# Kernel optimization log

Hardware: AMD Instinct MI355X
Metric: run time of the kernel (lower is better)

## Reference

```python
import jax, jax.numpy as jnp
import numpy as np

NUM = 8          # k_f*k_f - 1 neighbors (k_f = 3)
IDX_REF = 4      # center position index among the 9 kernel positions
EPS_TGASS = 1e-8


def _bilinear_gather(img, iy, ix):
    """img: (B,C,H,W); iy, ix: (B,N) absolute pixel coords.
    Bilinear sampling with zero padding. Matches both F.grid_sample
    (align_corners=True, padding_mode='zeros') and 1x1 modulated deform conv."""
    B, C, H, W = img.shape
    y0 = jnp.floor(iy)
    x0 = jnp.floor(ix)
    wy1 = iy - y0
    wx1 = ix - x0
    out = jnp.zeros((B, C, iy.shape[1]), img.dtype)
    for dy, dx, wy, wx in ((0.0, 0.0, 1.0 - wy1, 1.0 - wx1),
                           (0.0, 1.0, 1.0 - wy1, wx1),
                           (1.0, 0.0, wy1, 1.0 - wx1),
                           (1.0, 1.0, wy1, wx1)):
        yc = y0 + dy
        xc = x0 + dx
        valid = ((yc >= 0) & (yc <= H - 1) & (xc >= 0) & (xc <= W - 1)).astype(img.dtype)
        yi = jnp.clip(yc, 0, H - 1).astype(jnp.int32)
        xi = jnp.clip(xc, 0, W - 1).astype(jnp.int32)
        v = jax.vmap(lambda im, y, x: im[:, y, x])(img, yi, xi)  # (B,C,N)
        out = out + v * (wy * wx * valid)[:, None, :]
    return out


def setup_inputs() -> dict:
    key = jax.random.key(0)
    ks = jax.random.split(key, 5)
    B, Cg, H, W = 4, 16, 384, 384
    num, Cf = NUM, NUM  # cos-affinity path requires fea channels == num neighbors
    guidance = jax.random.normal(ks[0], (B, Cg, H, W), jnp.float32)
    gt_depth_conf = jax.random.uniform(ks[1], (B, 1, H, W), dtype=jnp.float32)
    tgtimg_fea = jax.random.normal(ks[2], (B, Cf, H, W), jnp.float32)
    # offset/affinity conv: 3*num output channels, 3x3 kernel; small init so offsets span a few pixels
    W_oa = jax.random.normal(ks[3], (3 * num, Cg, 3, 3), jnp.float32) * 0.05
    b_oa = jax.random.normal(ks[4], (3 * num,), jnp.float32) * 0.05
    aff_scale_const = jnp.full((1,), 0.5 * num, jnp.float32)  # TGASS: gamma * num
    return {"guidance": guidance, "gt_depth_conf": gt_depth_conf,
            "tgtimg_fea": tgtimg_fea, "W_oa": W_oa, "b_oa": b_oa,
            "aff_scale_const": aff_scale_const}


def reference(guidance, gt_depth_conf, tgtimg_fea, W_oa, b_oa, aff_scale_const):
    B, Cg, H, W = guidance.shape
    num = NUM

    # offset + affinity prediction conv (3x3, SAME padding)
    offset_aff = jax.lax.conv_general_dilated(
        guidance, W_oa, (1, 1), 'SAME',
        dimension_numbers=('NCHW', 'OIHW', 'NCHW')) + b_oa[None, :, None, None]
    o1, o2, aff = jnp.split(offset_aff, 3, axis=1)            # each (B,num,H,W)
    offset = jnp.concatenate([o1, o2], axis=1).reshape(B, num, 2, H, W)

    # ---- cos affinity: grid-sample gather of (detached) target features at offset locations
    fea = jax.lax.stop_gradient(tgtimg_fea)                   # (B,C,H,W), C == num
    C = fea.shape[1]
    rows = jnp.broadcast_to(jnp.arange(H, dtype=offset.dtype)[:, None], (H, W))
    cols = jnp.broadcast_to(jnp.arange(W, dtype=offset.dtype)[None, :], (H, W))
    xy = jnp.stack([rows, cols], -1)                          # (H,W,2)
    xy = jnp.repeat(xy, num, axis=-1)                         # (H,W,2*num): rows*num then cols*num
    xy_off = offset.reshape(B, 2 * num, H, W).transpose(0, 2, 3, 1) + xy  # (B,H,W,2*num)
    xy_off = xy_off.reshape(B, H, W, num, 2)
    gx = 2.0 * xy_off[..., 0] / (W - 1) - 1.0                 # grid x (width) coord
    gy = 2.0 * xy_off[..., 1] / (H - 1) - 1.0                 # grid y (height) coord
    ix = (gx + 1.0) * (W - 1) / 2.0
    iy = (gy + 1.0) * (H - 1) / 2.0
    sampled = _bilinear_gather(fea, iy.reshape(B, -1), ix.reshape(B, -1))  # (B,C,H*W*num)
    # torch does a raw .reshape of the (B,C,H,W*num) grid_sample output
    offset_feas = sampled.reshape(B, C, H, W * num).reshape(B, H, W, num, C)
    offset_feas = offset_feas.transpose(0, 3, 1, 2, 4)        # (B,num,H,W,C)
    cos_w = (offset_feas * fea[:, :, :, :, None]).sum(axis=1).transpose(0, 3, 1, 2)  # (B,num,H,W)
    aff = aff * cos_w                                         # use_aff=True

    # TGASS scaling
    aff = jnp.tanh(aff) / (aff_scale_const + EPS_TGASS)

    # full offset tensor with a zero offset inserted for the reference (center) pixel
    zero = jnp.zeros((B, 1, 2, H, W), offset.dtype)
    offset_full = jnp.concatenate([offset[:, :IDX_REF], zero, offset[:, IDX_REF:]], 1)
    offset_out = offset_full.reshape(B, -1, H, W)             # (B, 2*(num+1), H, W)

    # confidence propagation: 1x1 deformable sample of depth confidence (offsets detached)
    offs = jax.lax.stop_gradient(offset)                      # (B,num,2,H,W)
    dy = offs[:, :, 0]
    dx = offs[:, :, 1]
    sy = dy + jnp.arange(H, dtype=dy.dtype)[None, None, :, None]
    sx = dx + jnp.arange(W, dtype=dx.dtype)[None, None, None, :]
    conf = _bilinear_gather(gt_depth_conf, sy.reshape(B, -1), sx.reshape(B, -1))
    conf_aff = conf.reshape(B, num, H, W)
    aff = aff * conf_aff

    # affinity normalization (TGASS branch)
    aff_abs_sum = jnp.abs(aff).sum(axis=1, keepdims=True) + 1e-4
    aff_abs_sum = jnp.maximum(aff_abs_sum, 1.0)
    aff = aff / aff_abs_sum
    aff_ref = 1.0 - aff.sum(axis=1, keepdims=True)
    aff_full = jnp.concatenate([aff[:, :IDX_REF], aff_ref, aff[:, IDX_REF:]], 1)  # (B,9,H,W)
    aff_full = jax.nn.softmax(aff_full, axis=1)
    return (offset_out, aff_full)
```

## Files before the change

### kernel.cpp

```cpp
#include <hip/hip_runtime.h>

constexpr int Bn = 4, CG = 16, HH = 384, WW = 384;
constexpr int HWSZ = HH * WW;
constexpr int COUT = 24;
constexpr int TSX = 32, TSY = 16;

__global__ void wtrans_kernel(const float* __restrict__ Wc,
                              float* __restrict__ Wt) {
  int i = blockIdx.x * 256 + threadIdx.x;
  if (i < COUT * CG * 9) {
    int oc = i / (CG * 9), rem = i % (CG * 9);
    Wt[rem * COUT + oc] = Wc[i];
  }
}

__global__ __launch_bounds__(256) void conv5_kernel(
    const float* __restrict__ g, const float* __restrict__ Wt,
    const float* __restrict__ bc, float* __restrict__ out_off,
    float* __restrict__ affc, float* __restrict__ offT3f) {
  __shared__ float lds[8 * 18 * 34];
  int bi = blockIdx.x;
  int bx = (bi % (WW / TSX)) * TSX;
  int by = ((bi / (WW / TSX)) % (HH / TSY)) * TSY;
  int b = bi / ((WW / TSX) * (HH / TSY));
  const float* gb = g + (size_t)b * CG * HWSZ;

  int t = threadIdx.x;
  int tx = t & 15, ty = t >> 4;
  float acc0[COUT], acc1[COUT];
#pragma unroll
  for (int oc = 0; oc < COUT; ++oc) {
    float bv = bc[oc];
    acc0[oc] = bv;
    acc1[oc] = bv;
  }

  for (int half = 0; half < 2; ++half) {
    if (half) __syncthreads();
    for (int k = t; k < 8 * 18 * 34; k += 256) {
      int icl = k / 612, rem = k - 612 * icl;
      int y = rem / 34, x = rem - 34 * y;
      int gy = by + y - 1, gx = bx + x - 1;
      float v = (gy >= 0 && gy < HH && gx >= 0 && gx < WW)
                    ? gb[(half * 8 + icl) * HWSZ + gy * WW + gx]
                    : 0.f;
      lds[k] = v;
    }
    __syncthreads();

    for (int icl = 0; icl < 8; ++icl) {
      int ic = half * 8 + icl;
      const float* base = lds + icl * 612 + ty * 34 + 2 * tx;
      float vals[3][4];
#pragma unroll
      for (int r = 0; r < 3; ++r) {
        float2 v01 = *(const float2*)(base + r * 34);
        float2 v23 = *(const float2*)(base + r * 34 + 2);
        vals[r][0] = v01.x;
        vals[r][1] = v01.y;
        vals[r][2] = v23.x;
        vals[r][3] = v23.y;
      }
#pragma unroll
      for (int r = 0; r < 3; ++r) {
#pragma unroll
        for (int c3 = 0; c3 < 3; ++c3) {
          float va = vals[r][c3], vb = vals[r][c3 + 1];
          const float* wp = Wt + (ic * 9 + r * 3 + c3) * COUT;
#pragma unroll
          for (int oc = 0; oc < COUT; ++oc) {
            acc0[oc] += va * wp[oc];
            acc1[oc] += vb * wp[oc];
          }
        }
      }
    }
  }

  int p = (by + ty) * WW + bx + 2 * tx;
  float* ob = out_off + (size_t)b * 18 * HWSZ;
#pragma unroll
  for (int c = 0; c < 16; ++c) {
    int c18 = (c < 8) ? c : c + 2;
    *(float2*)(ob + c18 * HWSZ + p) = make_float2(acc0[c], acc1[c]);
  }
  *(float2*)(ob + 8 * HWSZ + p) = make_float2(0.f, 0.f);
  *(float2*)(ob + 9 * HWSZ + p) = make_float2(0.f, 0.f);
  float* ab = affc + (size_t)b * 8 * HWSZ;
#pragma unroll
  for (int c = 0; c < 8; ++c)
    *(float2*)(ab + c * HWSZ + p) = make_float2(acc0[16 + c], acc1[16 + c]);

  {
    int X0 = bx + 2 * tx;
    int m = X0 >> 3, j = X0 & 7;
    int Lp = by + ty;
    float* o3b = offT3f + (size_t)b * 16 * 48 * 384 * 4;
#pragma unroll
    for (int pl = 0; pl < 8; ++pl) {
      int cp = pl >> 1, sel = pl & 1;
      int q = sel * 2 + (j >> 2);
      size_t di = ((size_t)(cp * 4 + q) * 48 + m) * 384 + Lp;
      *(float2*)(o3b + di * 4 + (j & 3)) =
          make_float2(acc0[8 + pl], acc1[8 + pl]);
    }
  }
}

__device__ __forceinline__ float bilin_zero(const float* __restrict__ img,
                                            float iy, float ix) {
  float y0f = floorf(iy), x0f = floorf(ix);
  float wy1 = iy - y0f, wx1 = ix - x0f;
  int y0 = (int)y0f, x0 = (int)x0f;
  float acc = 0.f;
#pragma unroll
  for (int dy = 0; dy < 2; ++dy) {
    int yc = y0 + dy;
    bool vy = (yc >= 0) && (yc <= HH - 1);
    int yi = min(max(yc, 0), HH - 1);
    float wy = dy ? wy1 : 1.f - wy1;
#pragma unroll
    for (int dx = 0; dx < 2; ++dx) {
      int xc = x0 + dx;
      bool vx = (xc >= 0) && (xc <= WW - 1);
      int xi = min(max(xc, 0), WW - 1);
      float wx = dx ? wx1 : 1.f - wx1;
      float v = img[yi * WW + xi];
      acc += v * (wy * wx) * ((vy && vx) ? 1.f : 0.f);
    }
  }
  return acc;
}

__global__ __launch_bounds__(256, 4) void cw47h_kernel(
    const float* __restrict__ fea, const float4* __restrict__ offT3,
    float* __restrict__ cw4) {
  __shared__ float patch[64][68];
  __shared__ float sfea[8][64][5];
  __shared__ float scw[4][64][5];
  int t = threadIdx.x;
  int lane = t & 63, wv = t >> 6;
  int bi = blockIdx.x;
  int Lblk = bi % 6;  bi /= 6;
  int mblk = bi % 12; bi /= 12;
  int a = bi % 8, b = bi / 8;
  int m = mblk * 4 + wv;

  const float* feab = fea + (size_t)b * 8 * HWSZ;
  const float* imgA = feab + (size_t)a * HWSZ;
  int p_base = a * 18432 + 48 * (Lblk * 64) + mblk * 4;

  int R0 = 32 * mblk - 12;
  R0 = (R0 < 0) ? 0 : (R0 > 320 ? 320 : R0);

#pragma unroll
  for (int i = 0; i < 2; ++i) {
    int L = i * 256 + t;
    int j = L >> 6, Lpl = L & 63;
    float4 v = *(const float4*)(feab + (size_t)j * HWSZ + p_base + 48 * Lpl);
    sfea[j][Lpl][0] = v.x;
    sfea[j][Lpl][1] = v.y;
    sfea[j][Lpl][2] = v.z;
    sfea[j][Lpl][3] = v.w;
  }
  {
    int row = t >> 4, colq = t & 15;
#pragma unroll
    for (int pass = 0; pass < 4; ++pass) {
      int r = pass * 16 + row;
      float4 v = *(const float4*)(imgA + (R0 + r) * WW + R0 + 4 * colq);
      *(float4*)&patch[r][4 * colq] = v;
    }
  }
  __syncthreads();

  float feaj[8];
#pragma unroll
  for (int j = 0; j < 8; ++j) feaj[j] = sfea[j][lane][wv];

  const float4* o3 = offT3 + (size_t)b * 16 * 48 * 384;
  int recoff = m * 384 + (Lblk * 64 + lane);
  float qf = (float)(8 * m);

#pragma unroll
  for (int cp = 0; cp < 4; ++cp) {
    float4 dy0 = o3[(cp * 4 + 0) * 18432 + recoff];
    float4 dy1 = o3[(cp * 4 + 1) * 18432 + recoff];
    float4 dx0 = o3[(cp * 4 + 2) * 18432 + recoff];
    float4 dx1 = o3[(cp * 4 + 3) * 18432 + recoff];
    float dyv[8] = {dy0.x, dy0.y, dy0.z, dy0.w, dy1.x, dy1.y, dy1.z, dy1.w};
    float dxv[8] = {dx0.x, dx0.y, dx0.z, dx0.w, dx1.x, dx1.y, dx1.z, dx1.w};
    float s = 0.f;
#pragma unroll
    for (int j = 0; j < 8; ++j) {
      float iy = dxv[j] + qf + (float)j;
      float ix = dyv[j] + qf + (float)j;
      float y0f = floorf(iy), x0f = floorf(ix);
      int y0 = (int)y0f, x0 = (int)x0f;
      float fy = iy - y0f, fx = ix - x0f;
      float bv;
      if (y0 >= R0 && y0 <= R0 + 62 && x0 >= R0 && x0 <= R0 + 62) {
        int ry = y0 - R0, rx = x0 - R0;
        float v00 = patch[ry][rx], v01 = patch[ry][rx + 1];
        float v10 = patch[ry + 1][rx], v11 = patch[ry + 1][rx + 1];
        float wy0 = 1.f - fy, wx0 = 1.f - fx;
        bv = v00 * (wy0 * wx0) + v01 * (wy0 * fx) + v10 * (fy * wx0) +
             v11 * (fy * fx);
      } else {
        bv = bilin_zero(imgA, iy, ix);
      }
      s += feaj[j] * bv;
    }
    scw[cp][lane][wv] = s;
  }
  __syncthreads();

  {
    int cp = t >> 6, Lpl = t & 63;
    float4 v;
    v.x = scw[cp][Lpl][0];
    v.y = scw[cp][Lpl][1];
    v.z = scw[cp][Lpl][2];
    v.w = scw[cp][Lpl][3];
    *(float4*)(cw4 + (size_t)(b * 4 + cp) * HWSZ + p_base + 48 * Lpl) = v;
  }
}

__device__ __forceinline__ float fast_tanh(float x) {
  float ax = fabsf(x);
  float e = __expf(2.f * ax);
  float t = 1.f - 2.f * __builtin_amdgcn_rcpf(e + 1.f);
  return copysignf(t, x);
}

__global__ __launch_bounds__(256, 4) void fused5_kernel(
    const float* __restrict__ fea, const float* __restrict__ conf_img,
    const float* __restrict__ out_off, const float* __restrict__ affc,
    const float* __restrict__ cw4, const float* __restrict__ aff_scale,
    float* __restrict__ out_aff) {
  __shared__ float fpat[32][36];
  int t = threadIdx.x;
  unsigned idx0 = blockIdx.x * 256u;
  unsigned b = idx0 / (unsigned)HWSZ;
  unsigned pb0 = idx0 % (unsigned)HWSZ;
  unsigned a = (8u * pb0) / (unsigned)HWSZ;
  unsigned r0f = 8u * pb0 - a * (unsigned)HWSZ;
  int hrf = (int)(r0f / (unsigned)WW);
  int C0 = hrf - 12;
  C0 = (C0 < 0) ? 0 : (C0 > 352 ? 352 : C0);
  C0 &= ~3;

  const float* feab = fea + (size_t)b * 8 * HWSZ;
  const float* imgA = feab + (size_t)a * HWSZ;
  const float* cimg = conf_img + (size_t)b * HWSZ;

  unsigned p = pb0 + t;
  const float* offb = out_off + (size_t)b * 18 * HWSZ;
  const float* ab = affc + (size_t)b * 8 * HWSZ;

  float feaj[8];
#pragma unroll
  for (int j = 0; j < 8; ++j) feaj[j] = feab[j * HWSZ + p];
  float abv[8];
#pragma unroll
  for (int c = 0; c < 8; ++c) abv[c] = ab[c * HWSZ + p];
  float cw4v[4];
#pragma unroll
  for (int c = 0; c < 4; ++c) cw4v[c] = cw4[((size_t)b * 4 + c) * HWSZ + p];

  {
    int rr = t >> 3, cq = t & 7;
    *(float4*)&fpat[rr][4 * cq] =
        *(const float4*)(imgA + (C0 + rr) * WW + C0 + 4 * cq);
  }
  __syncthreads();

  unsigned h = p / (unsigned)WW, wcol = p % (unsigned)WW;
  unsigned r0 = 8u * p - a * (unsigned)HWSZ;
  unsigned hr = r0 / (unsigned)WW;
  float cb = (float)hr;

  float av[8];
#pragma unroll
  for (int c = 0; c < 4; ++c) {
    const float* dyp = offb + (2 * c) * HWSZ + r0;
    const float* dxp = offb + (2 * c + 1) * HWSZ + r0;
    float4 dy0 = *(const float4*)dyp, dy1 = *(const float4*)(dyp + 4);
    float4 dx0 = *(const float4*)dxp, dx1 = *(const float4*)(dxp + 4);
    float dyv[8] = {dy0.x, dy0.y, dy0.z, dy0.w, dy1.x, dy1.y, dy1.z, dy1.w};
    float dxv[8] = {dx0.x, dx0.y, dx0.z, dx0.w, dx1.x, dx1.y, dx1.z, dx1.w};
    float s = 0.f;
#pragma unroll
    for (int j = 0; j < 8; ++j) {
      float iy = dxv[j] + cb, ix = dyv[j] + cb;
      float y0f = floorf(iy), x0f = floorf(ix);
      int y0 = (int)y0f, x0 = (int)x0f;
      float fy = iy - y0f, fx = ix - x0f;
      float bv;
      if (y0 >= C0 && y0 <= C0 + 30 && x0 >= C0 && x0 <= C0 + 30) {
        int ry = y0 - C0, rx = x0 - C0;
        float wy0 = 1.f - fy, wx0 = 1.f - fx;
        bv = fpat[ry][rx] * (wy0 * wx0) + fpat[ry][rx + 1] * (wy0 * fx) +
             fpat[ry + 1][rx] * (fy * wx0) + fpat[ry + 1][rx + 1] * (fy * fx);
      } else {
        bv = bilin_zero(imgA, iy, ix);
      }
      s += feaj[j] * bv;
    }
    av[c] = abv[c] * s;
  }
#pragma unroll
  for (int c = 4; c < 8; ++c) av[c] = abv[c] * cw4v[c - 4];

  float cf[8];
#pragma unroll
  for (int c = 0; c < 8; ++c) {
    int chy = (c < 4) ? 2 * c : 2 * c + 2;
    float dy = offb[chy * HWSZ + p];
    float dx = offb[(chy + 1) * HWSZ + p];
    cf[c] = bilin_zero(cimg, dy + (float)h, dx + (float)wcol);
  }

  float invden = __builtin_amdgcn_rcpf(aff_scale[0] + 1e-8f);
  float tv8[8];
  float asum = 0.f;
#pragma unroll
  for (int c = 0; c < 8; ++c) {
    float tv = fast_tanh(av[c]) * invden * cf[c];
    tv8[c] = tv;
    asum += fabsf(tv);
  }
  asum += 1e-4f;
  asum = fmaxf(asum, 1.f);
  float inv_asum = __builtin_amdgcn_rcpf(asum);
  float ssum = 0.f;
#pragma unroll
  for (int c = 0; c < 8; ++c) {
    tv8[c] *= inv_asum;
    ssum += tv8[c];
  }

  float v9[9];
#pragma unroll
  for (int c = 0; c < 4; ++c) v9[c] = tv8[c];
  v9[4] = 1.f - ssum;
#pragma unroll
  for (int c = 4; c < 8; ++c) v9[c + 1] = tv8[c];

  float mx = v9[0];
#pragma unroll
  for (int i = 1; i < 9; ++i) mx = fmaxf(mx, v9[i]);
  float es = 0.f;
#pragma unroll
  for (int i = 0; i < 9; ++i) {
    v9[i] = __expf(v9[i] - mx);
    es += v9[i];
  }
  float inv = __builtin_amdgcn_rcpf(es);
  float* ob = out_aff + (size_t)b * 9 * HWSZ;
#pragma unroll
  for (int i = 0; i < 9; ++i) ob[i * HWSZ + p] = v9[i] * inv;
}

extern "C" void kernel_launch(void* const* d_in, const int* in_sizes, int n_in,
                              void* d_out, int out_size, void* d_ws,
                              size_t ws_size, hipStream_t stream) {
  const float* guidance = (const float*)d_in[0];
  const float* conf_img = (const float*)d_in[1];
  const float* fea = (const float*)d_in[2];
  const float* Wc = (const float*)d_in[3];
  const float* bc = (const float*)d_in[4];
  const float* ascale = (const float*)d_in[5];

  float* out = (float*)d_out;
  float* out_off = out;
  float* out_aff = out + (size_t)Bn * 18 * HWSZ;
  float* offT3f = out_aff;

  float* affc = (float*)d_ws;
  float* cw4 = affc + (size_t)Bn * 8 * HWSZ;
  float* Wt = cw4 + (size_t)Bn * 4 * HWSZ;

  wtrans_kernel<<<(COUT * CG * 9 + 255) / 256, 256, 0, stream>>>(Wc, Wt);

  int total = Bn * HWSZ;
  conv5_kernel<<<Bn * (HH / TSY) * (WW / TSX), 256, 0, stream>>>(
      guidance, Wt, bc, out_off, affc, offT3f);
  cw47h_kernel<<<total / 256, 256, 0, stream>>>(fea, (const float4*)offT3f,
                                                cw4);
  fused5_kernel<<<total / 256, 256, 0, stream>>>(fea, conf_img, out_off, affc,
                                                 cw4, ascale, out_aff);
}
```

Measured before the change: 154.1 us.

## Compute one pixel per thread in conv kernel with 16x16 tiles

The 3x3 offset/affinity convolution now has each thread produce a single output pixel instead of two horizontally adjacent ones. Tiles shrink from 32x16 to 16x16, doubling the grid. The accumulator registers are halved, which allows higher occupancy. In exchange, halo overhead per output grows, weight loads are no longer shared across two pixels, and stores become scalar rather than float2.

Measured after the change: 160.4 us. +4.1%, slower.

```diff
diff --git a/kernel.cpp b/kernel.cpp
--- a/kernel.cpp
+++ b/kernel.cpp
@@ -3,7 +3,6 @@
 constexpr int Bn = 4, CG = 16, HH = 384, WW = 384;
 constexpr int HWSZ = HH * WW;
 constexpr int COUT = 24;
-constexpr int TSX = 32, TSY = 16;
 
 __global__ void wtrans_kernel(const float* __restrict__ Wc,
                               float* __restrict__ Wt) {
@@ -14,32 +13,28 @@
   }
 }
 
-__global__ __launch_bounds__(256) void conv5_kernel(
+__global__ __launch_bounds__(256) void conv6_kernel(
     const float* __restrict__ g, const float* __restrict__ Wt,
     const float* __restrict__ bc, float* __restrict__ out_off,
     float* __restrict__ affc, float* __restrict__ offT3f) {
-  __shared__ float lds[8 * 18 * 34];
+  __shared__ float lds[8 * 18 * 18];
   int bi = blockIdx.x;
-  int bx = (bi % (WW / TSX)) * TSX;
-  int by = ((bi / (WW / TSX)) % (HH / TSY)) * TSY;
-  int b = bi / ((WW / TSX) * (HH / TSY));
+  int bx = (bi % 24) * 16;
+  int by = ((bi / 24) % 24) * 16;
+  int b = bi / 576;
   const float* gb = g + (size_t)b * CG * HWSZ;
 
   int t = threadIdx.x;
   int tx = t & 15, ty = t >> 4;
-  float acc0[COUT], acc1[COUT];
-#pragma unroll
-  for (int oc = 0; oc < COUT; ++oc) {
-    float bv = bc[oc];
-    acc0[oc] = bv;
-    acc1[oc] = bv;
-  }
+  float acc[COUT];
+#pragma unroll
+  for (int oc = 0; oc < COUT; ++oc) acc[oc] = bc[oc];
 
   for (int half = 0; half < 2; ++half) {
     if (half) __syncthreads();
-    for (int k = t; k < 8 * 18 * 34; k += 256) {
-      int icl = k / 612, rem = k - 612 * icl;
-      int y = rem / 34, x = rem - 34 * y;
+    for (int k = t; k < 8 * 324; k += 256) {
+      int icl = k / 324, rem = k - 324 * icl;
+      int y = rem / 18, x = rem - 18 * y;
       int gy = by + y - 1, gx = bx + x - 1;
       float v = (gy >= 0 && gy < HH && gx >= 0 && gx < WW)
                     ? gb[(half * 8 + icl) * HWSZ + gy * WW + gx]
@@ -50,49 +45,41 @@
 
     for (int icl = 0; icl < 8; ++icl) {
       int ic = half * 8 + icl;
-      const float* base = lds + icl * 612 + ty * 34 + 2 * tx;
-      float vals[3][4];
+      const float* base = lds + icl * 324 + ty * 18 + tx;
+      float vals[3][3];
 #pragma unroll
       for (int r = 0; r < 3; ++r) {
-        float2 v01 = *(const float2*)(base + r * 34);
-        float2 v23 = *(const float2*)(base + r * 34 + 2);
-        vals[r][0] = v01.x;
-        vals[r][1] = v01.y;
-        vals[r][2] = v23.x;
-        vals[r][3] = v23.y;
+#pragma unroll
+        for (int c = 0; c < 3; ++c) vals[r][c] = base[r * 18 + c];
       }
 #pragma unroll
       for (int r = 0; r < 3; ++r) {
 #pragma unroll
         for (int c3 = 0; c3 < 3; ++c3) {
-          float va = vals[r][c3], vb = vals[r][c3 + 1];
+          float va = vals[r][c3];
           const float* wp = Wt + (ic * 9 + r * 3 + c3) * COUT;
 #pragma unroll
-          for (int oc = 0; oc < COUT; ++oc) {
-            acc0[oc] += va * wp[oc];
-            acc1[oc] += vb * wp[oc];
-          }
+          for (int oc = 0; oc < COUT; ++oc) acc[oc] += va * wp[oc];
         }
       }
     }
   }
 
-  int p = (by + ty) * WW + bx + 2 * tx;
+  int p = (by + ty) * WW + bx + tx;
   float* ob = out_off + (size_t)b * 18 * HWSZ;
 #pragma unroll
   for (int c = 0; c < 16; ++c) {
     int c18 = (c < 8) ? c : c + 2;
-    *(float2*)(ob + c18 * HWSZ + p) = make_float2(acc0[c], acc1[c]);
-  }
-  *(float2*)(ob + 8 * HWSZ + p) = make_float2(0.f, 0.f);
-  *(float2*)(ob + 9 * HWSZ + p) = make_float2(0.f, 0.f);
+    ob[c18 * HWSZ + p] = acc[c];
+  }
+  ob[8 * HWSZ + p] = 0.f;
+  ob[9 * HWSZ + p] = 0.f;
   float* ab = affc + (size_t)b * 8 * HWSZ;
 #pragma unroll
-  for (int c = 0; c < 8; ++c)
-    *(float2*)(ab + c * HWSZ + p) = make_float2(acc0[16 + c], acc1[16 + c]);
+  for (int c = 0; c < 8; ++c) ab[c * HWSZ + p] = acc[16 + c];
 
   {
-    int X0 = bx + 2 * tx;
+    int X0 = bx + tx;
     int m = X0 >> 3, j = X0 & 7;
     int Lp = by + ty;
     float* o3b = offT3f + (size_t)b * 16 * 48 * 384 * 4;
@@ -101,8 +88,7 @@
       int cp = pl >> 1, sel = pl & 1;
       int q = sel * 2 + (j >> 2);
       size_t di = ((size_t)(cp * 4 + q) * 48 + m) * 384 + Lp;
-      *(float2*)(o3b + di * 4 + (j & 3)) =
-          make_float2(acc0[8 + pl], acc1[8 + pl]);
+      o3b[di * 4 + (j & 3)] = acc[8 + pl];
     }
   }
 }
@@ -384,8 +370,8 @@
   wtrans_kernel<<<(COUT * CG * 9 + 255) / 256, 256, 0, stream>>>(Wc, Wt);
 
   int total = Bn * HWSZ;
-  conv5_kernel<<<Bn * (HH / TSY) * (WW / TSX), 256, 0, stream>>>(
-      guidance, Wt, bc, out_off, affc, offT3f);
+  conv6_kernel<<<Bn * 24 * 24, 256, 0, stream>>>(guidance, Wt, bc, out_off,
+                                                 affc, offT3f);
   cw47h_kernel<<<total / 256, 256, 0, stream>>>(fea, (const float4*)offT3f,
                                                 cw4);
   fused5_kernel<<<total / 256, 256, 0, stream>>>(fea, conf_img, out_off, affc,
```
